# Optimization experiments

Measured on AMD Instinct MI355X. Metric: run time of the kernel, lower is better.

## Reference

```python
import jax, jax.numpy as jnp
import numpy as np

B, S, HID = 1, 2048, 4096
N_HEADS, N_KV_HEADS, HEAD_DIM = 32, 8, 128
ROPE_THETA = 10000.0


def rotate_half(x):
    # standard Llama rotate_half along last dim
    d = x.shape[-1] // 2
    return jnp.concatenate([-x[..., d:], x[..., :d]], axis=-1)


def rope_cos_sin(position_ids, dtype):
    # inv_freq: [head_dim/2]
    inv_freq = 1.0 / (ROPE_THETA ** (jnp.arange(0, HEAD_DIM, 2, dtype=jnp.float32) / HEAD_DIM))
    freqs = position_ids.astype(jnp.float32)[:, :, None] * inv_freq[None, None, :]  # [B,S,hd/2]
    emb = jnp.concatenate([freqs, freqs], axis=-1)  # [B,S,hd]
    return jnp.cos(emb).astype(dtype), jnp.sin(emb).astype(dtype)


def setup_inputs() -> dict:
    key = jax.random.key(0)
    ks = jax.random.split(key, 5)
    scale = 0.02
    return {
        "hidden_states": jax.random.normal(ks[0], (B, S, HID), dtype=jnp.float32),
        "position_ids": jnp.broadcast_to(jnp.arange(S, dtype=jnp.int32)[None, :], (B, S)),
        "Wq": jax.random.normal(ks[1], (N_HEADS * HEAD_DIM, HID), dtype=jnp.float32) * scale,
        "Wk": jax.random.normal(ks[2], (N_KV_HEADS * HEAD_DIM, HID), dtype=jnp.float32) * scale,
        "Wv": jax.random.normal(ks[3], (N_KV_HEADS * HEAD_DIM, HID), dtype=jnp.float32) * scale,
        "Wo": jax.random.normal(ks[4], (HID, HID), dtype=jnp.float32) * scale,
    }


def reference(hidden_states, position_ids, Wq, Wk, Wv, Wo):
    bsz, q_len, _ = hidden_states.shape
    n_rep = N_HEADS // N_KV_HEADS

    # projections (torch Linear: x @ W.T)
    q = (hidden_states @ Wq.T).reshape(bsz, q_len, N_HEADS, HEAD_DIM).transpose(0, 2, 1, 3)
    k = (hidden_states @ Wk.T).reshape(bsz, q_len, N_KV_HEADS, HEAD_DIM).transpose(0, 2, 1, 3)
    v = (hidden_states @ Wv.T).reshape(bsz, q_len, N_KV_HEADS, HEAD_DIM).transpose(0, 2, 1, 3)

    cos, sin = rope_cos_sin(position_ids, hidden_states.dtype)
    cos = cos[:, None, :, :]  # [B,1,S,hd]
    sin = sin[:, None, :, :]
    q = q * cos + rotate_half(q) * sin
    k = k * cos + rotate_half(k) * sin

    # GQA: repeat kv heads
    k = jnp.repeat(k, n_rep, axis=1)  # [B,nH,S,hd]
    v = jnp.repeat(v, n_rep, axis=1)

    scores = jnp.einsum("bhqd,bhkd->bhqk", q, k) / jnp.sqrt(jnp.asarray(HEAD_DIM, q.dtype))
    causal = jnp.tril(jnp.ones((q_len, q_len), dtype=bool))
    neg = jnp.asarray(jnp.finfo(jnp.float32).min, scores.dtype)
    scores = jnp.where(causal[None, None, :, :], scores, neg)

    attn = jax.nn.softmax(scores.astype(jnp.float32), axis=-1).astype(q.dtype)
    out = jnp.einsum("bhqk,bhkd->bhqd", attn, v)  # [B,nH,S,hd]
    out = out.transpose(0, 2, 1, 3).reshape(bsz, q_len, HID)
    return out @ Wo.T
```

## Files before the change

### kernel.cpp

```cpp
#include <hip/hip_runtime.h>

typedef __attribute__((ext_vector_type(4))) float f32x4;
typedef __attribute__((ext_vector_type(8))) __bf16 bf16x8;
typedef __attribute__((ext_vector_type(4))) unsigned short u16x4;

#define DEVI static __device__ __forceinline__
#define AS1 __attribute__((address_space(1)))
#define AS3 __attribute__((address_space(3)))

static constexpr int S_LEN = 2048;
static constexpr int HID   = 4096;
static constexpr int NH    = 32;
static constexpr int NKV   = 8;
static constexpr int HD    = 128;
static constexpr int NQKV  = HID + 2 * NKV * HD;

DEVI unsigned short f2bf(float f) {
  unsigned int u = __float_as_uint(f);
  u += 0x7FFFu + ((u >> 16) & 1u);
  return (unsigned short)(u >> 16);
}
DEVI float bf2f(unsigned short h) {
  return __uint_as_float(((unsigned int)h) << 16);
}

__global__ void cast_f32_bf16(const float* __restrict__ in,
                              unsigned short* __restrict__ out, int n4) {
  int i = blockIdx.x * 256 + threadIdx.x;
  if (i >= n4) return;
  float4 v = reinterpret_cast<const float4*>(in)[i];
  u16x4 o;
  o[0] = f2bf(v.x); o[1] = f2bf(v.y); o[2] = f2bf(v.z); o[3] = f2bf(v.w);
  reinterpret_cast<u16x4*>(out)[i] = o;
}

__global__ void rope_table(float2* __restrict__ tab) {
  int i = blockIdx.x * 256 + threadIdx.x;
  if (i >= S_LEN * 64) return;
  int j = i & 63, s = i >> 6;
  float inv = powf(10000.0f, -(float)j / 64.0f);
  float ang = (float)s * inv;
  tab[i] = make_float2(cosf(ang), sinf(ang));
}

__global__ void rope_all(unsigned short* __restrict__ Qb,
                         unsigned short* __restrict__ Kb,
                         const float2* __restrict__ tab) {
  const int totq = S_LEN * NH * 64;
  const int tot  = totq + S_LEN * NKV * 64;
  int i = blockIdx.x * 256 + threadIdx.x;
  if (i >= tot) return;
  unsigned short* X; int Hn, idx;
  if (i < totq) { X = Qb; Hn = NH; idx = i; }
  else          { X = Kb; Hn = NKV; idx = i - totq; }
  int j = idx & 63;
  int h = (idx >> 6) % Hn;
  int s = idx / (64 * Hn);
  float2 cs = tab[s * 64 + j];
  unsigned short* p = X + (size_t)s * Hn * HD + h * HD;
  float x1 = bf2f(p[j]);
  float x2 = bf2f(p[j + 64]);
  p[j]      = f2bf(x1 * cs.x - x2 * cs.y);
  p[j + 64] = f2bf(x2 * cs.x + x1 * cs.y);
}

__global__ __launch_bounds__(512, 2) void gemm_qkv256(
    const unsigned short* __restrict__ A,
    const unsigned short* __restrict__ B,
    unsigned short* __restrict__ Qb,
    unsigned short* __restrict__ Kb,
    unsigned short* __restrict__ Vt) {
  __shared__ __align__(16) unsigned short lds[2][32768];
  const int tid = threadIdx.x;
  const int lane = tid & 63, w = tid >> 6;
  const int wm = w >> 2, wn = w & 3;
  const int lr = lane & 15, lg = lane >> 4;
  const int bx = blockIdx.x, by = blockIdx.y;
  const int m0 = by * 256, n0 = bx * 256;
  const int Kd = HID;

  const int sAr = tid >> 3, sAp = tid & 7;
  const int sBn = tid >> 2, sBp = tid & 3;
  auto stageA = [&](int buf, int t, int band) {
    int row = band * 64 + sAr;
    __builtin_amdgcn_global_load_lds(
        (const AS1 void*)(A + (size_t)(m0 + row) * Kd + t * 64 + ((sAp ^ (row & 7)) * 8)),
        (AS3 void*)(&lds[buf][row * 64 + sAp * 8]), 16, 0, 0);
  };
  auto stageB = [&](int buf, int t, int kh, int hb) {
    int n = hb * 128 + sBn;
    __builtin_amdgcn_global_load_lds(
        (const AS1 void*)(B + (size_t)(n0 + n) * Kd + t * 64 + kh * 32 + ((sBp ^ ((n >> 1) & 3)) * 8)),
        (AS3 void*)(&lds[buf][16384 + kh * 8192 + n * 32 + sBp * 8]), 16, 0, 0);
  };

  const int aoff0 = (wm * 128 + lr) * 64 + ((lg ^ (lr & 7)) * 8);
  const int aoff1 = (wm * 128 + lr) * 64 + (((4 + lg) ^ (lr & 7)) * 8);
  const int boff  = 16384 + (wn * 64 + lr) * 32 + ((lg ^ ((lr >> 1) & 3)) * 8);

  f32x4 acc[8][4] = {};
  bf16x8 bgr[2][4];

#pragma unroll
  for (int b = 0; b < 4; ++b) { stageA(0, 0, b); stageA(1, 1, b); }
#pragma unroll
  for (int kh = 0; kh < 2; ++kh)
#pragma unroll
    for (int hb = 0; hb < 2; ++hb) { stageB(0, 0, kh, hb); stageB(1, 1, kh, hb); }
  asm volatile("s_waitcnt vmcnt(0)" ::: "memory");
  __builtin_amdgcn_s_barrier();

#define PHASE(BUF, MH, KH, LOADB, WAIT, ...)                                   \
  do {                                                                         \
    const unsigned short* ab = &lds[BUF][((KH) ? aoff1 : aoff0) + (MH) * 4096];\
    bf16x8 af0 = *reinterpret_cast<const bf16x8*>(ab);                         \
    bf16x8 af1 = *reinterpret_cast<const bf16x8*>(ab + 1024);                  \
    bf16x8 af2 = *reinterpret_cast<const bf16x8*>(ab + 2048);                  \
    bf16x8 af3 = *reinterpret_cast<const bf16x8*>(ab + 3072);                  \
    if (LOADB) {                                                               \
      const unsigned short* bb = &lds[BUF][boff + (KH) * 8192];                \
      bgr[KH][0] = *reinterpret_cast<const bf16x8*>(bb);                       \
      bgr[KH][1] = *reinterpret_cast<const bf16x8*>(bb + 512);                 \
      bgr[KH][2] = *reinterpret_cast<const bf16x8*>(bb + 1024);                \
      bgr[KH][3] = *reinterpret_cast<const bf16x8*>(bb + 1536);                \
    }                                                                          \
    __builtin_amdgcn_sched_barrier(0);                                         \
    __VA_ARGS__                                                                \
    asm volatile("s_waitcnt vmcnt(" WAIT ")" ::: "memory");                    \
    __builtin_amdgcn_s_barrier();                                              \
    asm volatile("s_waitcnt lgkmcnt(0)" ::: "memory");                         \
    __builtin_amdgcn_sched_barrier(0);                                         \
    __builtin_amdgcn_s_setprio(1);                                             \
    acc[(MH)*4+0][0] = __builtin_amdgcn_mfma_f32_16x16x32_bf16(af0, bgr[KH][0], acc[(MH)*4+0][0],0,0,0); \
    acc[(MH)*4+0][1] = __builtin_amdgcn_mfma_f32_16x16x32_bf16(af0, bgr[KH][1], acc[(MH)*4+0][1],0,0,0); \
    acc[(MH)*4+0][2] = __builtin_amdgcn_mfma_f32_16x16x32_bf16(af0, bgr[KH][2], acc[(MH)*4+0][2],0,0,0); \
    acc[(MH)*4+0][3] = __builtin_amdgcn_mfma_f32_16x16x32_bf16(af0, bgr[KH][3], acc[(MH)*4+0][3],0,0,0); \
    acc[(MH)*4+1][0] = __builtin_amdgcn_mfma_f32_16x16x32_bf16(af1, bgr[KH][0], acc[(MH)*4+1][0],0,0,0); \
    acc[(MH)*4+1][1] = __builtin_amdgcn_mfma_f32_16x16x32_bf16(af1, bgr[KH][1], acc[(MH)*4+1][1],0,0,0); \
    acc[(MH)*4+1][2] = __builtin_amdgcn_mfma_f32_16x16x32_bf16(af1, bgr[KH][2], acc[(MH)*4+1][2],0,0,0); \
    acc[(MH)*4+1][3] = __builtin_amdgcn_mfma_f32_16x16x32_bf16(af1, bgr[KH][3], acc[(MH)*4+1][3],0,0,0); \
    acc[(MH)*4+2][0] = __builtin_amdgcn_mfma_f32_16x16x32_bf16(af2, bgr[KH][0], acc[(MH)*4+2][0],0,0,0); \
    acc[(MH)*4+2][1] = __builtin_amdgcn_mfma_f32_16x16x32_bf16(af2, bgr[KH][1], acc[(MH)*4+2][1],0,0,0); \
    acc[(MH)*4+2][2] = __builtin_amdgcn_mfma_f32_16x16x32_bf16(af2, bgr[KH][2], acc[(MH)*4+2][2],0,0,0); \
    acc[(MH)*4+2][3] = __builtin_amdgcn_mfma_f32_16x16x32_bf16(af2, bgr[KH][3], acc[(MH)*4+2][3],0,0,0); \
    acc[(MH)*4+3][0] = __builtin_amdgcn_mfma_f32_16x16x32_bf16(af3, bgr[KH][0], acc[(MH)*4+3][0],0,0,0); \
    acc[(MH)*4+3][1] = __builtin_amdgcn_mfma_f32_16x16x32_bf16(af3, bgr[KH][1], acc[(MH)*4+3][1],0,0,0); \
    acc[(MH)*4+3][2] = __builtin_amdgcn_mfma_f32_16x16x32_bf16(af3, bgr[KH][2], acc[(MH)*4+3][2],0,0,0); \
    acc[(MH)*4+3][3] = __builtin_amdgcn_mfma_f32_16x16x32_bf16(af3, bgr[KH][3], acc[(MH)*4+3][3],0,0,0); \
    __builtin_amdgcn_s_setprio(0);                                             \
    __builtin_amdgcn_s_barrier();                                              \
  } while (0)

  for (int i = 0; i < 31; ++i) {
    const int t = 2 * i;
    const bool nf = (i != 0);
    PHASE(0, 0, 0, 1, "6", if (nf) { stageB(1, t + 1, 0, 0); stageB(1, t + 1, 0, 1); });
    PHASE(0, 0, 1, 1, "6", if (nf) { stageB(1, t + 1, 1, 0); stageB(1, t + 1, 1, 1); });
    PHASE(0, 1, 0, 0, "6", if (nf) { stageA(1, t + 1, 1); stageA(1, t + 1, 3); });
    PHASE(0, 1, 1, 0, "6", { stageB(0, t + 2, 0, 0); stageB(0, t + 2, 0, 1); });
    PHASE(1, 0, 0, 1, "6", { stageA(0, t + 2, 0); stageA(0, t + 2, 2); });
    PHASE(1, 0, 1, 1, "6", { stageB(0, t + 2, 1, 0); stageB(0, t + 2, 1, 1); });
    PHASE(1, 1, 0, 0, "6", { stageA(0, t + 2, 1); stageA(0, t + 2, 3); });
    PHASE(1, 1, 1, 0, "6", { stageA(1, t + 3, 0); stageA(1, t + 3, 2); });
  }
  {
    const int t = 62;
    PHASE(0, 0, 0, 1, "6", { stageB(1, t + 1, 0, 0); stageB(1, t + 1, 0, 1); });
    PHASE(0, 0, 1, 1, "6", { stageB(1, t + 1, 1, 0); stageB(1, t + 1, 1, 1); });
    PHASE(0, 1, 0, 0, "6", { stageA(1, t + 1, 1); stageA(1, t + 1, 3); });
    PHASE(0, 1, 1, 0, "4", ;);
    PHASE(1, 0, 0, 1, "2", ;);
    PHASE(1, 0, 1, 1, "0", ;);
    PHASE(1, 1, 0, 0, "0", ;);
    PHASE(1, 1, 1, 0, "0", ;);
  }
#undef PHASE

#pragma unroll
  for (int ar = 0; ar < 8; ++ar) {
#pragma unroll
    for (int fc = 0; fc < 4; ++fc) {
      const int gcol = n0 + wn * 64 + fc * 16 + lr;
      const int growb = m0 + wm * 128 + (ar >> 2) * 64 + (ar & 3) * 16 + lg * 4;
      if (bx < 16) {
#pragma unroll
        for (int rr = 0; rr < 4; ++rr)
          Qb[(size_t)(growb + rr) * HID + gcol] = f2bf(acc[ar][fc][rr]);
      } else if (bx < 20) {
#pragma unroll
        for (int rr = 0; rr < 4; ++rr)
          Kb[(size_t)(growb + rr) * (NKV * HD) + (gcol - HID)] = f2bf(acc[ar][fc][rr]);
      } else {
        u16x4 o4;
#pragma unroll
        for (int rr = 0; rr < 4; ++rr) o4[rr] = f2bf(acc[ar][fc][rr]);
        *reinterpret_cast<u16x4*>(
            &Vt[(size_t)(gcol - HID - NKV * HD) * S_LEN + growb]) = o4;
      }
    }
  }
}

__global__ __launch_bounds__(512, 2) void gemm_o256(
    const unsigned short* __restrict__ A,
    const unsigned short* __restrict__ B,
    float* __restrict__ C) {
  __shared__ __align__(16) unsigned short lds[2][24576];
  const int tid = threadIdx.x;
  const int lane = tid & 63, w = tid >> 6;
  const int wm = w >> 2, wn = w & 3;
  const int lr = lane & 15, lg = lane >> 4;
  const int m0 = blockIdx.y * 128, n0 = blockIdx.x * 256;
  const int Kd = HID;

  const int sAr = tid >> 3, sAp = tid & 7;
  const int sBn = tid >> 2, sBp = tid & 3;
  auto stA = [&](int buf, int t, int unit) {
    int row = unit * 64 + sAr;
    __builtin_amdgcn_global_load_lds(
        (const AS1 void*)(A + (size_t)(m0 + row) * Kd + t * 64 + ((sAp ^ (row & 7)) * 8)),
        (AS3 void*)(&lds[buf][row * 64 + sAp * 8]), 16, 0, 0);
  };
  auto stB = [&](int buf, int t, int kh, int hb) {
    int n = hb * 128 + sBn;
    __builtin_amdgcn_global_load_lds(
        (const AS1 void*)(B + (size_t)(n0 + n) * Kd + t * 64 + kh * 32 + ((sBp ^ ((n >> 1) & 3)) * 8)),
        (AS3 void*)(&lds[buf][8192 + kh * 8192 + n * 32 + sBp * 8]), 16, 0, 0);
  };

  const int aoffk0 = (wm * 64 + lr) * 64 + ((lg ^ (lr & 7)) * 8);
  const int aoffk1 = (wm * 64 + lr) * 64 + (((4 + lg) ^ (lr & 7)) * 8);
  const int boff   = 8192 + (wn * 64 + lr) * 32 + ((lg ^ ((lr >> 1) & 3)) * 8);

  f32x4 acc[4][4] = {};
  bf16x8 bgr[4];

#pragma unroll
  for (int u = 0; u < 2; ++u) { stA(0, 0, u); stA(1, 1, u); }
#pragma unroll
  for (int kh = 0; kh < 2; ++kh)
#pragma unroll
    for (int hb = 0; hb < 2; ++hb) { stB(0, 0, kh, hb); stB(1, 1, kh, hb); }
  asm volatile("s_waitcnt vmcnt(0)" ::: "memory");
  __builtin_amdgcn_s_barrier();

#define OPHASE(BUF, KH, MH, LOADB, WAITOP, ...)                                \
  do {                                                                         \
    const unsigned short* ab = &lds[BUF][((KH) ? aoffk1 : aoffk0) + (MH) * 2048];\
    bf16x8 af0 = *reinterpret_cast<const bf16x8*>(ab);                         \
    bf16x8 af1 = *reinterpret_cast<const bf16x8*>(ab + 1024);                  \
    if (LOADB) {                                                               \
      const unsigned short* bb = &lds[BUF][boff + (KH) * 8192];                \
      bgr[0] = *reinterpret_cast<const bf16x8*>(bb);                           \
      bgr[1] = *reinterpret_cast<const bf16x8*>(bb + 512);                     \
      bgr[2] = *reinterpret_cast<const bf16x8*>(bb + 1024);                    \
      bgr[3] = *reinterpret_cast<const bf16x8*>(bb + 1536);                    \
    }                                                                          \
    __builtin_amdgcn_sched_barrier(0);                                         \
    __VA_ARGS__                                                                \
    WAITOP                                                                     \
    __builtin_amdgcn_s_barrier();                                              \
    asm volatile("s_waitcnt lgkmcnt(0)" ::: "memory");                         \
    __builtin_amdgcn_sched_barrier(0);                                         \
    __builtin_amdgcn_s_setprio(1);                                             \
    acc[(MH)*2+0][0] = __builtin_amdgcn_mfma_f32_16x16x32_bf16(af0, bgr[0], acc[(MH)*2+0][0],0,0,0); \
    acc[(MH)*2+0][1] = __builtin_amdgcn_mfma_f32_16x16x32_bf16(af0, bgr[1], acc[(MH)*2+0][1],0,0,0); \
    acc[(MH)*2+0][2] = __builtin_amdgcn_mfma_f32_16x16x32_bf16(af0, bgr[2], acc[(MH)*2+0][2],0,0,0); \
    acc[(MH)*2+0][3] = __builtin_amdgcn_mfma_f32_16x16x32_bf16(af0, bgr[3], acc[(MH)*2+0][3],0,0,0); \
    acc[(MH)*2+1][0] = __builtin_amdgcn_mfma_f32_16x16x32_bf16(af1, bgr[0], acc[(MH)*2+1][0],0,0,0); \
    acc[(MH)*2+1][1] = __builtin_amdgcn_mfma_f32_16x16x32_bf16(af1, bgr[1], acc[(MH)*2+1][1],0,0,0); \
    acc[(MH)*2+1][2] = __builtin_amdgcn_mfma_f32_16x16x32_bf16(af1, bgr[2], acc[(MH)*2+1][2],0,0,0); \
    acc[(MH)*2+1][3] = __builtin_amdgcn_mfma_f32_16x16x32_bf16(af1, bgr[3], acc[(MH)*2+1][3],0,0,0); \
    __builtin_amdgcn_s_setprio(0);                                             \
    __builtin_amdgcn_s_barrier();                                              \
  } while (0)

#define VM2 asm volatile("s_waitcnt vmcnt(2)" ::: "memory");
#define VM0 asm volatile("s_waitcnt vmcnt(0)" ::: "memory");
#define NOW

  for (int i = 0; i < 31; ++i) {
    const int t = 2 * i;
    const bool nf = (i != 0);
    OPHASE(0, 0, 0, 1, NOW, if (nf) { stA(1, t + 1, 0); stA(1, t + 1, 1);
                                      stB(1, t + 1, 1, 0); stB(1, t + 1, 1, 1); });
    OPHASE(0, 0, 1, 0, NOW, ;);
    OPHASE(0, 1, 0, 1, NOW, { stB(0, t + 2, 0, 0); stB(0, t + 2, 0, 1); });
    OPHASE(0, 1, 1, 0, VM2, ;);
    OPHASE(1, 0, 0, 1, NOW, { stA(0, t + 2, 0); stA(0, t + 2, 1);
                              stB(0, t + 2, 1, 0); stB(0, t + 2, 1, 1); });
    OPHASE(1, 0, 1, 0, NOW, ;);
    OPHASE(1, 1, 0, 1, NOW, { stB(1, t + 3, 0, 0); stB(1, t + 3, 0, 1); });
    OPHASE(1, 1, 1, 0, VM2, ;);
  }
  {
    const int t = 62;
    OPHASE(0, 0, 0, 1, NOW, { stA(1, t + 1, 0); stA(1, t + 1, 1);
                              stB(1, t + 1, 1, 0); stB(1, t + 1, 1, 1); });
    OPHASE(0, 0, 1, 0, NOW, ;);
    OPHASE(0, 1, 0, 1, NOW, ;);
    OPHASE(0, 1, 1, 0, VM0, ;);
    OPHASE(1, 0, 0, 1, NOW, ;);
    OPHASE(1, 0, 1, 0, NOW, ;);
    OPHASE(1, 1, 0, 1, NOW, ;);
    OPHASE(1, 1, 1, 0, NOW, ;);
  }
#undef OPHASE
#undef VM2
#undef VM0
#undef NOW

#pragma unroll
  for (int ar = 0; ar < 4; ++ar) {
#pragma unroll
    for (int fc = 0; fc < 4; ++fc) {
      const int gcol = n0 + wn * 64 + fc * 16 + lr;
      const int growb = m0 + wm * 64 + ar * 16 + lg * 4;
#pragma unroll
      for (int rr = 0; rr < 4; ++rr)
        C[(size_t)(growb + rr) * HID + gcol] = acc[ar][fc][rr];
    }
  }
}

__global__ __launch_bounds__(512, 4) void attn_kernel(
    const unsigned short* __restrict__ Q,
    const unsigned short* __restrict__ Kb,
    const unsigned short* __restrict__ Vt,
    unsigned short* __restrict__ O) {
  __shared__ __align__(16) unsigned short sK[2][64 * 128];
  __shared__ __align__(16) unsigned short sV[2][128 * 64];
  const int tid = threadIdx.x;
  const int lane = tid & 63, w = tid >> 6;
  const int lr = lane & 15, lg = lane >> 4;
  const int qt = (int)gridDim.x - 1 - (int)blockIdx.x;
  const int h = blockIdx.y, kvh = h >> 2;
  const int q0 = qt * 128, qw = q0 + w * 16;
  const int KVS = NKV * HD;

  bf16x8 qf[4];
#pragma unroll
  for (int ks = 0; ks < 4; ++ks)
    qf[ks] = *reinterpret_cast<const bf16x8*>(
        &Q[(size_t)(qw + lr) * HID + h * HD + ks * 32 + lg * 8]);

  f32x4 ao[8] = {};
  float mrun = -INFINITY, lrun = 0.f;
  const float S2 = 0.12751745f;
  const int ntiles = 2 * qt + 2;

  auto stage = [&](int b, int kv0) {
#pragma unroll
    for (int i = 0; i < 2; ++i) {
      int off = (tid + i * 512) * 8;
      int r = off >> 7, c = (off >> 3) & 15;
      __builtin_amdgcn_global_load_lds(
          (const AS1 void*)(Kb + (size_t)(kv0 + r) * KVS + kvh * HD + ((c ^ (r & 15)) * 8)),
          (AS3 void*)(&sK[b][off]), 16, 0, 0);
    }
#pragma unroll
    for (int i = 0; i < 2; ++i) {
      int off = (tid + i * 512) * 8;
      int r = off >> 6, c = (off >> 3) & 7;
      __builtin_amdgcn_global_load_lds(
          (const AS1 void*)(Vt + (size_t)(kvh * HD + r) * S_LEN + kv0 + ((c ^ (r & 7)) * 8)),
          (AS3 void*)(&sV[b][off]), 16, 0, 0);
    }
  };

  stage(0, 0);
  __syncthreads();
  int cur = 0;

  for (int t = 0; t < ntiles; ++t) {
    const int kv0 = t * 64;
    if (t + 1 < ntiles) stage(cur ^ 1, kv0 + 64);

    if (kv0 <= qw + 15) {
      f32x4 sacc[4] = {};
      __builtin_amdgcn_s_setprio(1);
#pragma unroll
      for (int kt = 0; kt < 4; ++kt)
#pragma unroll
        for (int ks = 0; ks < 4; ++ks) {
          int elem = (kt * 16 + lr) * 128 + (((4 * ks + lg) ^ lr) * 8);
          bf16x8 kf = *reinterpret_cast<const bf16x8*>(&sK[cur][elem]);
          sacc[kt] = __builtin_amdgcn_mfma_f32_16x16x32_bf16(kf, qf[ks], sacc[kt], 0, 0, 0);
        }
      __builtin_amdgcn_s_setprio(0);

      const bool needMask = (kv0 + 63 > qw);
      const int qg = qw + lr;
      float p[16];
      float tmax = -INFINITY;
#pragma unroll
      for (int kt = 0; kt < 4; ++kt)
#pragma unroll
        for (int r = 0; r < 4; ++r) {
          float v = sacc[kt][r] * S2;
          if (needMask && (kv0 + kt * 16 + lg * 4 + r > qg)) v = -INFINITY;
          p[kt * 4 + r] = v;
          tmax = fmaxf(tmax, v);
        }
      tmax = fmaxf(tmax, __shfl_xor(tmax, 16));
      tmax = fmaxf(tmax, __shfl_xor(tmax, 32));
      if (!__all(tmax <= mrun + 8.0f)) {
        float mnew = fmaxf(mrun, tmax);
        float corr = exp2f(mrun - mnew);
        lrun *= corr;
#pragma unroll
        for (int dt = 0; dt < 8; ++dt) ao[dt] *= corr;
        mrun = mnew;
      }
      float rs = 0.f;
#pragma unroll
      for (int i = 0; i < 16; ++i) { p[i] = exp2f(p[i] - mrun); rs += p[i]; }
      rs += __shfl_xor(rs, 16);
      rs += __shfl_xor(rs, 32);
      lrun += rs;

      unsigned int bfrag[2][4];
#pragma unroll
      for (int g = 0; g < 2; ++g) {
        unsigned int Au = (unsigned)f2bf(p[8 * g + 0]) | ((unsigned)f2bf(p[8 * g + 1]) << 16);
        unsigned int Bu = (unsigned)f2bf(p[8 * g + 2]) | ((unsigned)f2bf(p[8 * g + 3]) << 16);
        unsigned int Cu = (unsigned)f2bf(p[8 * g + 4]) | ((unsigned)f2bf(p[8 * g + 5]) << 16);
        unsigned int Du = (unsigned)f2bf(p[8 * g + 6]) | ((unsigned)f2bf(p[8 * g + 7]) << 16);
        int s0 = (lg & 1) * 2;
        int src0 = lr + 16 * s0, src1 = src0 + 16;
        bool hi = lg >= 2;
        int a0 = __shfl((int)Au, src0), c0 = __shfl((int)Cu, src0);
        int b0 = __shfl((int)Bu, src0), d0 = __shfl((int)Du, src0);
        int a1 = __shfl((int)Au, src1), c1 = __shfl((int)Cu, src1);
        int b1 = __shfl((int)Bu, src1), d1 = __shfl((int)Du, src1);
        bfrag[g][0] = hi ? (unsigned)c0 : (unsigned)a0;
        bfrag[g][1] = hi ? (unsigned)d0 : (unsigned)b0;
        bfrag[g][2] = hi ? (unsigned)c1 : (unsigned)a1;
        bfrag[g][3] = hi ? (unsigned)d1 : (unsigned)b1;
      }

      __builtin_amdgcn_s_setprio(1);
#pragma unroll
      for (int g = 0; g < 2; ++g)
#pragma unroll
        for (int dt = 0; dt < 8; ++dt) {
          int d = dt * 16 + lr;
          int elem = d * 64 + (((4 * g + lg) ^ (lr & 7)) * 8);
          bf16x8 vf = *reinterpret_cast<const bf16x8*>(&sV[cur][elem]);
          ao[dt] = __builtin_amdgcn_mfma_f32_16x16x32_bf16(
              vf, *reinterpret_cast<const bf16x8*>(&bfrag[g]), ao[dt], 0, 0, 0);
        }
      __builtin_amdgcn_s_setprio(0);
    }

    __syncthreads();
    cur ^= 1;
  }

  float inv = 1.0f / lrun;
  int qrow = qw + lr;
#pragma unroll
  for (int dt = 0; dt < 8; ++dt) {
    u16x4 o4;
#pragma unroll
    for (int r = 0; r < 4; ++r) o4[r] = f2bf(ao[dt][r] * inv);
    *reinterpret_cast<u16x4*>(&O[(size_t)qrow * HID + h * HD + dt * 16 + lg * 4]) = o4;
  }
}

extern "C" void kernel_launch(void* const* d_in, const int* in_sizes, int n_in,
                              void* d_out, int out_size, void* d_ws, size_t ws_size,
                              hipStream_t stream) {
  const float* hs = (const float*)d_in[0];
  const float* Wq = (const float*)d_in[2];
  const float* Wk = (const float*)d_in[3];
  const float* Wv = (const float*)d_in[4];
  const float* Wo = (const float*)d_in[5];

  unsigned short* ws = (unsigned short*)d_ws;
  size_t off = 0;
  unsigned short* H16  = ws + off; off += (size_t)S_LEN * HID;
  unsigned short* Wcat = ws + off; off += (size_t)NQKV * HID;
  unsigned short* Qb   = ws + off; off += (size_t)S_LEN * HID;
  unsigned short* Kb   = ws + off; off += (size_t)S_LEN * NKV * HD;
  unsigned short* Vt   = ws + off; off += (size_t)S_LEN * NKV * HD;
  float2* tab = (float2*)(ws + off); off += (size_t)S_LEN * 64 * 2 * 2;

  auto cast = [&](const float* src, unsigned short* dst, size_t n) {
    int n4 = (int)(n / 4);
    cast_f32_bf16<<<(n4 + 255) / 256, 256, 0, stream>>>(src, dst, n4);
  };

  rope_table<<<(S_LEN * 64 + 255) / 256, 256, 0, stream>>>(tab);
  cast(hs, H16, (size_t)S_LEN * HID);
  cast(Wq, Wcat, (size_t)HID * HID);
  cast(Wk, Wcat + (size_t)HID * HID, (size_t)NKV * HD * HID);
  cast(Wv, Wcat + (size_t)(HID + NKV * HD) * HID, (size_t)NKV * HD * HID);

  gemm_qkv256<<<dim3(NQKV / 256, S_LEN / 256), 512, 0, stream>>>(
      H16, Wcat, Qb, Kb, Vt);

  cast(Wo, Wcat, (size_t)HID * HID);

  {
    int tot = S_LEN * NH * 64 + S_LEN * NKV * 64;
    rope_all<<<(tot + 255) / 256, 256, 0, stream>>>(Qb, Kb, tab);
  }

  attn_kernel<<<dim3(S_LEN / 128, NH), 512, 0, stream>>>(Qb, Kb, Vt, H16);

  gemm_o256<<<dim3(HID / 256, S_LEN / 128), 512, 0, stream>>>(
      H16, Wcat, (float*)d_out);
}
```

Measured before the change: 360.1 us.

## Retile QKV GEMM to 128x192 blocks with simpler double-buffered pipeline

Replaces the 256x256 QKV projection GEMM tile with a 128x192 tile, giving a 32x16 grid (512 blocks) instead of 24x8 (192 blocks) so the work spreads better across the CUs. LDS use per block drops, and the launch bound now asks for up to 4 blocks per CU. The fine-grained staggered prefetch schedule is replaced by a coarser one that issues a whole k-tile prefetch at once and waits with vmcnt(0) every four phases. Smaller tiles lower arithmetic intensity and add global traffic, and the full waits may expose memory latency.

```diff
diff --git a/kernel.cpp b/kernel.cpp
--- a/kernel.cpp
+++ b/kernel.cpp
@@ -64,136 +64,118 @@
   p[j + 64] = f2bf(x2 * cs.x + x1 * cs.y);
 }
 
-__global__ __launch_bounds__(512, 2) void gemm_qkv256(
+__global__ __launch_bounds__(512, 4) void gemm_qkv192(
     const unsigned short* __restrict__ A,
     const unsigned short* __restrict__ B,
     unsigned short* __restrict__ Qb,
     unsigned short* __restrict__ Kb,
     unsigned short* __restrict__ Vt) {
-  __shared__ __align__(16) unsigned short lds[2][32768];
+  __shared__ __align__(16) unsigned short lds[2][20480];
   const int tid = threadIdx.x;
   const int lane = tid & 63, w = tid >> 6;
   const int wm = w >> 2, wn = w & 3;
   const int lr = lane & 15, lg = lane >> 4;
-  const int bx = blockIdx.x, by = blockIdx.y;
-  const int m0 = by * 256, n0 = bx * 256;
+  const int n0 = blockIdx.x * 192, m0 = blockIdx.y * 128;
   const int Kd = HID;
 
   const int sAr = tid >> 3, sAp = tid & 7;
-  const int sBn = tid >> 2, sBp = tid & 3;
-  auto stageA = [&](int buf, int t, int band) {
-    int row = band * 64 + sAr;
+  auto stA = [&](int buf, int t, int u) {
+    int row = u * 64 + sAr;
     __builtin_amdgcn_global_load_lds(
         (const AS1 void*)(A + (size_t)(m0 + row) * Kd + t * 64 + ((sAp ^ (row & 7)) * 8)),
         (AS3 void*)(&lds[buf][row * 64 + sAp * 8]), 16, 0, 0);
   };
-  auto stageB = [&](int buf, int t, int kh, int hb) {
-    int n = hb * 128 + sBn;
+  auto stB = [&](int buf, int t, int v) {
+    int row = v * 64 + sAr;
     __builtin_amdgcn_global_load_lds(
-        (const AS1 void*)(B + (size_t)(n0 + n) * Kd + t * 64 + kh * 32 + ((sBp ^ ((n >> 1) & 3)) * 8)),
-        (AS3 void*)(&lds[buf][16384 + kh * 8192 + n * 32 + sBp * 8]), 16, 0, 0);
-  };
-
-  const int aoff0 = (wm * 128 + lr) * 64 + ((lg ^ (lr & 7)) * 8);
-  const int aoff1 = (wm * 128 + lr) * 64 + (((4 + lg) ^ (lr & 7)) * 8);
-  const int boff  = 16384 + (wn * 64 + lr) * 32 + ((lg ^ ((lr >> 1) & 3)) * 8);
-
-  f32x4 acc[8][4] = {};
-  bf16x8 bgr[2][4];
-
-#pragma unroll
-  for (int b = 0; b < 4; ++b) { stageA(0, 0, b); stageA(1, 1, b); }
-#pragma unroll
-  for (int kh = 0; kh < 2; ++kh)
-#pragma unroll
-    for (int hb = 0; hb < 2; ++hb) { stageB(0, 0, kh, hb); stageB(1, 1, kh, hb); }
+        (const AS1 void*)(B + (size_t)(n0 + row) * Kd + t * 64 + ((sAp ^ (row & 7)) * 8)),
+        (AS3 void*)(&lds[buf][8192 + row * 64 + sAp * 8]), 16, 0, 0);
+  };
+
+  const int arow = (wm * 64 + lr) * 64;
+  const int brow = 8192 + (wn * 48 + lr) * 64;
+  const int ck0 = ((lg) ^ (lr & 7)) * 8;
+  const int ck1 = ((4 + lg) ^ (lr & 7)) * 8;
+
+  f32x4 acc[4][3] = {};
+  bf16x8 bgr[3];
+
+#pragma unroll
+  for (int u = 0; u < 2; ++u) { stA(0, 0, u); stA(1, 1, u); }
+#pragma unroll
+  for (int v = 0; v < 3; ++v) { stB(0, 0, v); stB(1, 1, v); }
   asm volatile("s_waitcnt vmcnt(0)" ::: "memory");
   __builtin_amdgcn_s_barrier();
 
-#define PHASE(BUF, MH, KH, LOADB, WAIT, ...)                                   \
+#define QPHASE(BUF, KH, MH, LOADB, WAITOP, ...)                                \
   do {                                                                         \
-    const unsigned short* ab = &lds[BUF][((KH) ? aoff1 : aoff0) + (MH) * 4096];\
+    const int ck = (KH) ? ck1 : ck0;                                           \
+    const unsigned short* ab = &lds[BUF][arow + (MH) * 2048 + ck];             \
     bf16x8 af0 = *reinterpret_cast<const bf16x8*>(ab);                         \
     bf16x8 af1 = *reinterpret_cast<const bf16x8*>(ab + 1024);                  \
-    bf16x8 af2 = *reinterpret_cast<const bf16x8*>(ab + 2048);                  \
-    bf16x8 af3 = *reinterpret_cast<const bf16x8*>(ab + 3072);                  \
     if (LOADB) {                                                               \
-      const unsigned short* bb = &lds[BUF][boff + (KH) * 8192];                \
-      bgr[KH][0] = *reinterpret_cast<const bf16x8*>(bb);                       \
-      bgr[KH][1] = *reinterpret_cast<const bf16x8*>(bb + 512);                 \
-      bgr[KH][2] = *reinterpret_cast<const bf16x8*>(bb + 1024);                \
-      bgr[KH][3] = *reinterpret_cast<const bf16x8*>(bb + 1536);                \
+      const unsigned short* bb = &lds[BUF][brow + ck];                         \
+      bgr[0] = *reinterpret_cast<const bf16x8*>(bb);                           \
+      bgr[1] = *reinterpret_cast<const bf16x8*>(bb + 1024);                    \
+      bgr[2] = *reinterpret_cast<const bf16x8*>(bb + 2048);                    \
     }                                                                          \
     __builtin_amdgcn_sched_barrier(0);                                         \
     __VA_ARGS__                                                                \
-    asm volatile("s_waitcnt vmcnt(" WAIT ")" ::: "memory");                    \
+    WAITOP                                                                     \
     __builtin_amdgcn_s_barrier();                                              \
     asm volatile("s_waitcnt lgkmcnt(0)" ::: "memory");                         \
     __builtin_amdgcn_sched_barrier(0);                                         \
     __builtin_amdgcn_s_setprio(1);                                             \
-    acc[(MH)*4+0][0] = __builtin_amdgcn_mfma_f32_16x16x32_bf16(af0, bgr[KH][0], acc[(MH)*4+0][0],0,0,0); \
-    acc[(MH)*4+0][1] = __builtin_amdgcn_mfma_f32_16x16x32_bf16(af0, bgr[KH][1], acc[(MH)*4+0][1],0,0,0); \
-    acc[(MH)*4+0][2] = __builtin_amdgcn_mfma_f32_16x16x32_bf16(af0, bgr[KH][2], acc[(MH)*4+0][2],0,0,0); \
-    acc[(MH)*4+0][3] = __builtin_amdgcn_mfma_f32_16x16x32_bf16(af0, bgr[KH][3], acc[(MH)*4+0][3],0,0,0); \
-    acc[(MH)*4+1][0] = __builtin_amdgcn_mfma_f32_16x16x32_bf16(af1, bgr[KH][0], acc[(MH)*4+1][0],0,0,0); \
-    acc[(MH)*4+1][1] = __builtin_amdgcn_mfma_f32_16x16x32_bf16(af1, bgr[KH][1], acc[(MH)*4+1][1],0,0,0); \
-    acc[(MH)*4+1][2] = __builtin_amdgcn_mfma_f32_16x16x32_bf16(af1, bgr[KH][2], acc[(MH)*4+1][2],0,0,0); \
-    acc[(MH)*4+1][3] = __builtin_amdgcn_mfma_f32_16x16x32_bf16(af1, bgr[KH][3], acc[(MH)*4+1][3],0,0,0); \
-    acc[(MH)*4+2][0] = __builtin_amdgcn_mfma_f32_16x16x32_bf16(af2, bgr[KH][0], acc[(MH)*4+2][0],0,0,0); \
-    acc[(MH)*4+2][1] = __builtin_amdgcn_mfma_f32_16x16x32_bf16(af2, bgr[KH][1], acc[(MH)*4+2][1],0,0,0); \
-    acc[(MH)*4+2][2] = __builtin_amdgcn_mfma_f32_16x16x32_bf16(af2, bgr[KH][2], acc[(MH)*4+2][2],0,0,0); \
-    acc[(MH)*4+2][3] = __builtin_amdgcn_mfma_f32_16x16x32_bf16(af2, bgr[KH][3], acc[(MH)*4+2][3],0,0,0); \
-    acc[(MH)*4+3][0] = __builtin_amdgcn_mfma_f32_16x16x32_bf16(af3, bgr[KH][0], acc[(MH)*4+3][0],0,0,0); \
-    acc[(MH)*4+3][1] = __builtin_amdgcn_mfma_f32_16x16x32_bf16(af3, bgr[KH][1], acc[(MH)*4+3][1],0,0,0); \
-    acc[(MH)*4+3][2] = __builtin_amdgcn_mfma_f32_16x16x32_bf16(af3, bgr[KH][2], acc[(MH)*4+3][2],0,0,0); \
-    acc[(MH)*4+3][3] = __builtin_amdgcn_mfma_f32_16x16x32_bf16(af3, bgr[KH][3], acc[(MH)*4+3][3],0,0,0); \
+    acc[(MH)*2+0][0] = __builtin_amdgcn_mfma_f32_16x16x32_bf16(af0, bgr[0], acc[(MH)*2+0][0],0,0,0); \
+    acc[(MH)*2+0][1] = __builtin_amdgcn_mfma_f32_16x16x32_bf16(af0, bgr[1], acc[(MH)*2+0][1],0,0,0); \
+    acc[(MH)*2+0][2] = __builtin_amdgcn_mfma_f32_16x16x32_bf16(af0, bgr[2], acc[(MH)*2+0][2],0,0,0); \
+    acc[(MH)*2+1][0] = __builtin_amdgcn_mfma_f32_16x16x32_bf16(af1, bgr[0], acc[(MH)*2+1][0],0,0,0); \
+    acc[(MH)*2+1][1] = __builtin_amdgcn_mfma_f32_16x16x32_bf16(af1, bgr[1], acc[(MH)*2+1][1],0,0,0); \
+    acc[(MH)*2+1][2] = __builtin_amdgcn_mfma_f32_16x16x32_bf16(af1, bgr[2], acc[(MH)*2+1][2],0,0,0); \
     __builtin_amdgcn_s_setprio(0);                                             \
     __builtin_amdgcn_s_barrier();                                              \
   } while (0)
 
-  for (int i = 0; i < 31; ++i) {
+#define QVM0 asm volatile("s_waitcnt vmcnt(0)" ::: "memory");
+#define QNOW
+
+  for (int i = 0; i < 32; ++i) {
     const int t = 2 * i;
-    const bool nf = (i != 0);
-    PHASE(0, 0, 0, 1, "6", if (nf) { stageB(1, t + 1, 0, 0); stageB(1, t + 1, 0, 1); });
-    PHASE(0, 0, 1, 1, "6", if (nf) { stageB(1, t + 1, 1, 0); stageB(1, t + 1, 1, 1); });
-    PHASE(0, 1, 0, 0, "6", if (nf) { stageA(1, t + 1, 1); stageA(1, t + 1, 3); });
-    PHASE(0, 1, 1, 0, "6", { stageB(0, t + 2, 0, 0); stageB(0, t + 2, 0, 1); });
-    PHASE(1, 0, 0, 1, "6", { stageA(0, t + 2, 0); stageA(0, t + 2, 2); });
-    PHASE(1, 0, 1, 1, "6", { stageB(0, t + 2, 1, 0); stageB(0, t + 2, 1, 1); });
-    PHASE(1, 1, 0, 0, "6", { stageA(0, t + 2, 1); stageA(0, t + 2, 3); });
-    PHASE(1, 1, 1, 0, "6", { stageA(1, t + 3, 0); stageA(1, t + 3, 2); });
-  }
-  {
-    const int t = 62;
-    PHASE(0, 0, 0, 1, "6", { stageB(1, t + 1, 0, 0); stageB(1, t + 1, 0, 1); });
-    PHASE(0, 0, 1, 1, "6", { stageB(1, t + 1, 1, 0); stageB(1, t + 1, 1, 1); });
-    PHASE(0, 1, 0, 0, "6", { stageA(1, t + 1, 1); stageA(1, t + 1, 3); });
-    PHASE(0, 1, 1, 0, "4", ;);
-    PHASE(1, 0, 0, 1, "2", ;);
-    PHASE(1, 0, 1, 1, "0", ;);
-    PHASE(1, 1, 0, 0, "0", ;);
-    PHASE(1, 1, 1, 0, "0", ;);
-  }
-#undef PHASE
-
-#pragma unroll
-  for (int ar = 0; ar < 8; ++ar) {
-#pragma unroll
-    for (int fc = 0; fc < 4; ++fc) {
-      const int gcol = n0 + wn * 64 + fc * 16 + lr;
-      const int growb = m0 + wm * 128 + (ar >> 2) * 64 + (ar & 3) * 16 + lg * 4;
-      if (bx < 16) {
+    const bool nf = (i != 0), nl = (i != 31);
+    QPHASE(0, 0, 0, 1, QNOW, if (nf) { stA(1, t + 1, 0); stA(1, t + 1, 1);
+                                       stB(1, t + 1, 0); stB(1, t + 1, 1); stB(1, t + 1, 2); });
+    QPHASE(0, 0, 1, 0, QNOW, ;);
+    QPHASE(0, 1, 0, 1, QNOW, ;);
+    QPHASE(0, 1, 1, 0, QVM0, ;);
+    QPHASE(1, 0, 0, 1, QNOW, if (nl) { stA(0, t + 2, 0); stA(0, t + 2, 1);
+                                       stB(0, t + 2, 0); stB(0, t + 2, 1); stB(0, t + 2, 2); });
+    QPHASE(1, 0, 1, 0, QNOW, ;);
+    QPHASE(1, 1, 0, 1, QNOW, ;);
+    QPHASE(1, 1, 1, 0, QVM0, ;);
+  }
+#undef QPHASE
+#undef QVM0
+#undef QNOW
+
+#pragma unroll
+  for (int ar = 0; ar < 4; ++ar) {
+#pragma unroll
+    for (int c = 0; c < 3; ++c) {
+      const int gcolb = n0 + wn * 48 + c * 16;
+      const int gcol = gcolb + lr;
+      const int growb = m0 + wm * 64 + ar * 16 + lg * 4;
+      if (gcolb < HID) {
 #pragma unroll
         for (int rr = 0; rr < 4; ++rr)
-          Qb[(size_t)(growb + rr) * HID + gcol] = f2bf(acc[ar][fc][rr]);
-      } else if (bx < 20) {
+          Qb[(size_t)(growb + rr) * HID + gcol] = f2bf(acc[ar][c][rr]);
+      } else if (gcolb < HID + NKV * HD) {
 #pragma unroll
         for (int rr = 0; rr < 4; ++rr)
-          Kb[(size_t)(growb + rr) * (NKV * HD) + (gcol - HID)] = f2bf(acc[ar][fc][rr]);
+          Kb[(size_t)(growb + rr) * (NKV * HD) + (gcol - HID)] = f2bf(acc[ar][c][rr]);
       } else {
         u16x4 o4;
 #pragma unroll
-        for (int rr = 0; rr < 4; ++rr) o4[rr] = f2bf(acc[ar][fc][rr]);
+        for (int rr = 0; rr < 4; ++rr) o4[rr] = f2bf(acc[ar][c][rr]);
         *reinterpret_cast<u16x4*>(
             &Vt[(size_t)(gcol - HID - NKV * HD) * S_LEN + growb]) = o4;
       }
@@ -497,7 +479,7 @@
   cast(Wk, Wcat + (size_t)HID * HID, (size_t)NKV * HD * HID);
   cast(Wv, Wcat + (size_t)(HID + NKV * HD) * HID, (size_t)NKV * HD * HID);
 
-  gemm_qkv256<<<dim3(NQKV / 256, S_LEN / 256), 512, 0, stream>>>(
+  gemm_qkv192<<<dim3(NQKV / 192, S_LEN / 128), 512, 0, stream>>>(
       H16, Wcat, Qb, Kb, Vt);
 
   cast(Wo, Wcat, (size_t)HID * HID);
```

After: 350.4 us. 1.03x faster.
